# Kernel tuning notes

Measured on AMD Instinct MI355X. Metric: run time of the kernel, lower is better.

The kernel has to match this reference:

```python
import jax, jax.numpy as jnp
import numpy as np

B, S, D, F, E, DT, K = 4, 2048, 1024, 4096, 8, 256, 2


def setup_inputs() -> dict:
    key = jax.random.key(0)
    ks = jax.random.split(key, 8)
    scale_g = 1.0 / np.sqrt(D)
    scale_t = 1.0 / np.sqrt(DT)
    scale_1 = 1.0 / np.sqrt(D)
    scale_2 = 1.0 / np.sqrt(F)
    return {
        "inputs": jax.random.normal(ks[0], (B, S, D), dtype=jnp.float32),
        "task_param": jax.random.normal(ks[1], (B, 1, DT), dtype=jnp.float32),
        "Wg_in": jax.random.normal(ks[2], (D, E), dtype=jnp.float32) * scale_g,
        "bg_in": jnp.zeros((E,), dtype=jnp.float32),
        "Wg_task": jax.random.normal(ks[3], (DT, E), dtype=jnp.float32) * scale_t,
        "bg_task": jnp.zeros((E,), dtype=jnp.float32),
        "alpha": jnp.float32(0.5),
        "W1": jax.random.normal(ks[4], (E, D, F), dtype=jnp.float32) * scale_1,
        "b1": jnp.zeros((E, F), dtype=jnp.float32),
        "W2": jax.random.normal(ks[5], (E, F, D), dtype=jnp.float32) * scale_2,
        "b2": jnp.zeros((E, D), dtype=jnp.float32),
    }


def reference(inputs, task_param, Wg_in, bg_in, Wg_task, bg_task, alpha, W1, b1, W2, b2):
    # Gating: blend input-gate and task-gate logits ([B,1,E] broadcasts over S)
    input_logits = jnp.einsum('bsd,de->bse', inputs, Wg_in) + bg_in
    task_logits = jnp.einsum('btd,de->bte', task_param, Wg_task) + bg_task
    gate_logits = (1.0 - alpha) * input_logits + alpha * task_logits  # [B,S,E]

    topk_vals, selected = jax.lax.top_k(gate_logits, K)  # [B,S,K]

    # Load-balancing auxiliary loss (float32 softmax, as in the original)
    weights_softmax = jax.nn.softmax(gate_logits.astype(jnp.float32), axis=-1).astype(inputs.dtype)
    average_weight = jnp.mean(weights_softmax, axis=(0, 1))  # [E]
    onehot = jax.nn.one_hot(selected, E, dtype=inputs.dtype)  # [B,S,K,E]
    average_count = jnp.mean(onehot.sum(axis=2), axis=(0, 1))  # [E]
    l_aux = jnp.mean(average_weight * average_count) * E

    # Combine weights: softmax over the top-k gate values
    w = jax.nn.softmax(topk_vals.astype(jnp.float32), axis=-1).astype(inputs.dtype)  # [B,S,K]

    # Dense expert compute (same math as the per-expert gather/scatter loop)
    h = jax.nn.silu(jnp.einsum('bsd,edf->ebsf', inputs, W1) + b1[:, None, None, :])  # [E,B,S,F]
    expert_out = jnp.einsum('ebsf,efd->ebsd', h, W2) + b2[:, None, None, :]          # [E,B,S,D]

    picked = jnp.einsum('bske,ebsd->bskd', onehot, expert_out)  # [B,S,K,D]
    results = jnp.einsum('bsk,bskd->bsd', w, picked)            # [B,S,D]
    return results, l_aux.astype(jnp.float32)
```

## Files before the change

kernel.cpp:

```cpp
#include <hip/hip_runtime.h>

#define T_TOK 8192
#define D_DIM 1024
#define F_DIM 4096
#define E_EXP 8
#define DT_DIM 256
#define GBLK 256

#define A_XB   0u
#define A_WT   16777216u
#define A_H    83886080u
#define A_Y    226492416u
#define A_META 262144000u
#define A_W2T  262428928u
#define W2T_NEED (262428928ull + 67108864ull)
#define MO_FILL   0
#define MO_PB     64
#define MO_NT     128
#define MO_PARTP  256
#define MO_PARTC  8448
#define MO_TILEE  16640
#define MO_TILERB 17664
#define MO_ROUTEE 18688
#define MO_ROUTEW 84224
#define MO_TSLOT  149760
#define MO_PTOK   215296
#define META_BYTES 284928

using bf16x8 = __attribute__((ext_vector_type(8))) short;
using f32x4  = __attribute__((ext_vector_type(4))) float;
typedef unsigned short u16;

__device__ __forceinline__ u16 f2bf(float f) {
  union { float f; unsigned u; } v; v.f = f;
  unsigned r = v.u + 0x7FFFu + ((v.u >> 16) & 1u);
  return (u16)(r >> 16);
}
__device__ __forceinline__ float bf2f(u16 h) {
  union { unsigned u; float f; } v; v.u = ((unsigned)h) << 16; return v.f;
}
__device__ __forceinline__ void gload16(const void* gsrc, void* ldst) {
  __builtin_amdgcn_global_load_lds(
      (const __attribute__((address_space(1))) void*)gsrc,
      (__attribute__((address_space(3))) void*)ldst, 16, 0, 0);
}

__device__ __forceinline__ void tcvt64_body(const float* __restrict__ src,
                                            u16* __restrict__ dst, int R, int C,
                                            int e, int rb, int cb, char* smem) {
  u16 (*tile)[65] = (u16(*)[65])smem;
  size_t off = (size_t)e * R * C;
  int t = threadIdx.x;
  int r = t >> 4, cq = (t & 15) << 2;
#pragma unroll
  for (int k = 0; k < 4; k++) {
    int rr = r + k * 16;
    float4 v = *(const float4*)(src + off + (size_t)(rb + rr) * C + cb + cq);
    tile[rr][cq] = f2bf(v.x);
    tile[rr][cq + 1] = f2bf(v.y);
    tile[rr][cq + 2] = f2bf(v.z);
    tile[rr][cq + 3] = f2bf(v.w);
  }
  __syncthreads();
  int r4 = (t & 15) << 2, c0 = t >> 4;
#pragma unroll
  for (int j = 0; j < 4; j++) {
    int c = c0 + j * 16;
    ushort4 o;
    o.x = tile[r4][c]; o.y = tile[r4 + 1][c];
    o.z = tile[r4 + 2][c]; o.w = tile[r4 + 3][c];
    *(ushort4*)(dst + off + (size_t)(cb + c) * R + rb + r4) = o;
  }
}

__global__ __launch_bounds__(256) void prep(
    const float* __restrict__ X, const float* __restrict__ TP,
    const float* __restrict__ Wg, const float* __restrict__ bg,
    const float* __restrict__ Wt, const float* __restrict__ bgt,
    const float* __restrict__ alphaP,
    const float* __restrict__ W1,
    u16* __restrict__ Xb, u16* __restrict__ W1T, int* meta) {
  __shared__ char smem[41216];
  int bid = blockIdx.x;
  if (bid >= GBLK) {
    int loc = bid - GBLK;
    int e = loc >> 10, t10 = loc & 1023;
    tcvt64_body(W1, W1T, D_DIM, F_DIM, e, (t10 & 15) << 6, (t10 >> 4) << 6, smem);
    return;
  }
  float* WgT = (float*)smem;
  float* WtT = (float*)(smem + 32768);
  float* wsP = (float*)(smem + 40960);
  int*   wsC = (int*)(smem + 41088);
  int tid = threadIdx.x;
  for (int i = tid; i < E_EXP * D_DIM; i += 256) { int d = i >> 3, e = i & 7; WgT[e * D_DIM + d] = Wg[i]; }
  for (int i = tid; i < E_EXP * DT_DIM; i += 256) { int d = i >> 3, e = i & 7; WtT[e * DT_DIM + d] = Wt[i]; }
  __syncthreads();
  int lane = tid & 63, wid = tid >> 6;
  int tb = bid * 32;
  int b = tb >> 11;
  float alpha = alphaP[0];

  float tac[8] = {};
#pragma unroll
  for (int i = 0; i < 4; i++) {
    int d = lane + i * 64;
    float x = TP[b * DT_DIM + d];
#pragma unroll
    for (int e = 0; e < 8; e++) tac[e] += x * WtT[e * DT_DIM + d];
  }
  for (int off = 32; off > 0; off >>= 1)
#pragma unroll
    for (int e = 0; e < 8; e++) tac[e] += __shfl_xor(tac[e], off);
  float tl[8];
#pragma unroll
  for (int e = 0; e < 8; e++) tl[e] = alpha * (tac[e] + bgt[e]);

  float psum[8] = {};
  int   cnt[8] = {};
  for (int i = 0; i < 8; i++) {
    int t = tb + wid * 8 + i;
    const float* xr = X + (size_t)t * D_DIM;
    float acc[8] = {};
    u16 xb[16];
#pragma unroll 4
    for (int j = 0; j < 16; j++) {
      int d = lane + j * 64;
      float x = xr[d];
      xb[j] = f2bf(x);
#pragma unroll
      for (int e = 0; e < 8; e++) acc[e] += x * WgT[e * D_DIM + d];
    }
#pragma unroll
    for (int j = 0; j < 16; j++) Xb[(size_t)t * D_DIM + lane + j * 64] = xb[j];
    for (int off = 32; off > 0; off >>= 1)
#pragma unroll
      for (int e = 0; e < 8; e++) acc[e] += __shfl_xor(acc[e], off);
    float gl[8];
#pragma unroll
    for (int e = 0; e < 8; e++) gl[e] = (1.f - alpha) * (acc[e] + bg[e]) + tl[e];
    int e1 = 0;
#pragma unroll
    for (int e = 1; e < 8; e++) if (gl[e] > gl[e1]) e1 = e;
    int es = (e1 == 0) ? 1 : 0;
#pragma unroll
    for (int e = 0; e < 8; e++) if (e != e1 && gl[e] > gl[es]) es = e;
    float mx = gl[0];
#pragma unroll
    for (int e = 1; e < 8; e++) mx = fmaxf(mx, gl[e]);
    float pe[8], se = 0.f;
#pragma unroll
    for (int e = 0; e < 8; e++) { pe[e] = __expf(gl[e] - mx); se += pe[e]; }
    float inv = 1.f / se;
    if (lane == 0) {
#pragma unroll
      for (int e = 0; e < 8; e++) psum[e] += pe[e] * inv;
      cnt[e1]++; cnt[es]++;
      float w1 = 1.f / (1.f + __expf(gl[es] - gl[e1]));
      meta[MO_ROUTEE / 4 + 2 * t] = e1;
      meta[MO_ROUTEE / 4 + 2 * t + 1] = es;
      ((float*)meta)[MO_ROUTEW / 4 + 2 * t] = w1;
      ((float*)meta)[MO_ROUTEW / 4 + 2 * t + 1] = 1.f - w1;
    }
  }
  if (lane == 0) {
#pragma unroll
    for (int e = 0; e < 8; e++) { wsP[wid * 8 + e] = psum[e]; wsC[wid * 8 + e] = cnt[e]; }
  }
  __syncthreads();
  if (tid < 8) {
    float p = wsP[tid] + wsP[8 + tid] + wsP[16 + tid] + wsP[24 + tid];
    int   c = wsC[tid] + wsC[8 + tid] + wsC[16 + tid] + wsC[24 + tid];
    ((float*)meta)[MO_PARTP / 4 + bid * 8 + tid] = p;
    meta[MO_PARTC / 4 + bid * 8 + tid] = c;
  }
}

__global__ __launch_bounds__(256) void tcvt2k(const float* __restrict__ W2,
                                              u16* __restrict__ W2T) {
  __shared__ char smem[8448];
  int loc = blockIdx.x;
  int e = loc >> 10, t10 = loc & 1023;
  tcvt64_body(W2, W2T, F_DIM, D_DIM, e, (t10 >> 4) << 6, (t10 & 15) << 6, smem);
}

__global__ void plan(int* meta, float* out) {
  __shared__ float sp[8];
  __shared__ int   sc[8];
  int tid = threadIdx.x;
  if (blockIdx.x != 0) return;
  if (tid < 8) {
    const float* pp = (const float*)meta + MO_PARTP / 4;
    const int*   pc = meta + MO_PARTC / 4;
    float p = 0.f; int c = 0;
    for (int b = 0; b < GBLK; b++) { p += pp[b * 8 + tid]; c += pc[b * 8 + tid]; }
    sp[tid] = p; sc[tid] = c;
    meta[MO_FILL / 4 + tid] = 0;
  }
  int* ptok = meta + MO_PTOK / 4;
  for (int i = tid; i < 17408; i += 64) ptok[i] = 0;
  __syncthreads();
  if (tid == 0) {
    int* pb = meta + MO_PB / 4;
    int* tileE = meta + MO_TILEE / 4;
    int* tileRB = meta + MO_TILERB / 4;
    int base = 0, nt = 0;
    float la = 0.f;
    for (int e = 0; e < 8; e++) {
      int n = sc[e];
      pb[e] = base;
      int ntl = (n + 127) >> 7;
      for (int i = 0; i < ntl; i++) { tileE[nt] = e; tileRB[nt] = base + (i << 7); nt++; }
      base += ntl << 7;
      la += (sp[e] * (1.f / 8192.f)) * ((float)n * (1.f / 8192.f));
    }
    pb[8] = base;
    meta[MO_NT / 4] = nt;
    out[T_TOK * D_DIM] = la;
  }
}

__global__ __launch_bounds__(256) void fillk(int* meta) {
  int t = blockIdx.x * 256 + threadIdx.x;
  int lane = threadIdx.x & 63;
  int* pb = meta + MO_PB / 4;
  int* fl = meta + MO_FILL / 4;
  int* ptok = meta + MO_PTOK / 4;
  int* ts = meta + MO_TSLOT / 4;
  unsigned long long lmask = (1ull << lane) - 1;
#pragma unroll
  for (int k = 0; k < 2; k++) {
    int e = meta[MO_ROUTEE / 4 + 2 * t + k];
    int slot = 0;
    for (int ee = 0; ee < 8; ee++) {
      unsigned long long mask = __ballot(e == ee);
      if (e == ee) {
        int low = __ffsll((long long)mask) - 1;
        int pre = __popcll(mask & lmask);
        int base = 0;
        if (lane == low) base = atomicAdd(&fl[ee], __popcll(mask));
        base = __shfl(base, low);
        slot = pb[ee] + base + pre;
      }
    }
    ptok[slot] = t;
    ts[2 * t + k] = slot;
  }
}


#define BUFA(i) ((char*)smem + (i) * 16384)
#define BUFB(i) ((char*)smem + (i) * 16384 + 8192)

__global__ __launch_bounds__(256) void gemm1(
    const u16* __restrict__ Xb, const u16* __restrict__ W1T,
    const float* __restrict__ b1, u16* __restrict__ H,
    const float* __restrict__ W2, u16* __restrict__ W2T,
    const int* __restrict__ meta) {
  __shared__ char smem[49152];
  if (blockIdx.x >= 4352) {
    int loc = blockIdx.x - 4352;
    int e = loc >> 10, t10 = loc & 1023;
    tcvt64_body(W2, W2T, F_DIM, D_DIM, e, (t10 >> 4) << 6, (t10 & 15) << 6, smem);
    return;
  }
  int xcd = blockIdx.x & 7, loc = blockIdx.x >> 3;
  int bt = loc >> 2;
  int cb = (xcd * 4 + (loc & 3)) * 128;
  int nt = meta[MO_NT / 4];
  if (bt >= nt) return;
  int e = meta[MO_TILEE / 4 + bt];
  int rb = meta[MO_TILERB / 4 + bt];
  const int* ptok = meta + MO_PTOK / 4;

  int tid = threadIdx.x, lane = tid & 63, wid = tid >> 6;
  int wr = wid >> 1, wc = wid & 1;
  int r0 = tid >> 2;
  int c0 = (((tid & 3) ^ ((r0 >> 1) & 3)) << 3);
  int tok0 = ptok[rb + r0];
  int tok1 = ptok[rb + r0 + 64];
  const u16* gA0 = Xb + (size_t)tok0 * D_DIM + c0;
  const u16* gA1 = Xb + (size_t)tok1 * D_DIM + c0;
  const u16* gB0 = W1T + ((size_t)e * F_DIM + cb + r0) * D_DIM + c0;
  const u16* gB1 = gB0 + (size_t)64 * D_DIM;

#define STAGE_G1(buf, k0)                                  \
  {                                                        \
    gload16(gA0 + (k0), BUFA(buf) + wid * 1024);           \
    gload16(gA1 + (k0), BUFA(buf) + 4096 + wid * 1024);    \
    gload16(gB0 + (k0), BUFB(buf) + wid * 1024);           \
    gload16(gB1 + (k0), BUFB(buf) + 4096 + wid * 1024);    \
  }

  f32x4 acc[4][4] = {};
  int kb = (((lane >> 4) ^ (((lane & 15) >> 1) & 3)) << 3);
  int ra = wr * 64 + (lane & 15);
  int rn = wc * 64 + (lane & 15);
  STAGE_G1(0, 0)
  STAGE_G1(1, 32)
  int cur = 0;
  for (int kt = 0; kt < 32; kt++) {
    if (kt + 1 < 32)
      asm volatile("s_waitcnt vmcnt(4) lgkmcnt(0)" ::: "memory");
    else
      asm volatile("s_waitcnt vmcnt(0) lgkmcnt(0)" ::: "memory");
    __builtin_amdgcn_sched_barrier(0);
    __builtin_amdgcn_s_barrier();
    int nxt = cur + 2; if (nxt >= 3) nxt -= 3;
    if (kt + 2 < 32) STAGE_G1(nxt, (kt + 2) * 32)
    const short* pA = (const short*)BUFA(cur);
    const short* pB = (const short*)BUFB(cur);
    bf16x8 af[4], bfr[4];
#pragma unroll
    for (int m = 0; m < 4; m++)
      af[m] = *(const bf16x8*)((const char*)pA + ((ra + m * 16) * 32 + kb) * 2);
#pragma unroll
    for (int n = 0; n < 4; n++)
      bfr[n] = *(const bf16x8*)((const char*)pB + ((rn + n * 16) * 32 + kb) * 2);
    __builtin_amdgcn_s_setprio(1);
#pragma unroll
    for (int m = 0; m < 4; m++)
#pragma unroll
      for (int n = 0; n < 4; n++)
        acc[m][n] = __builtin_amdgcn_mfma_f32_16x16x32_bf16(af[m], bfr[n], acc[m][n], 0, 0, 0);
    __builtin_amdgcn_s_setprio(0);
    cur = cur + 1 == 3 ? 0 : cur + 1;
  }
  int rbase = wr * 64 + ((lane >> 4) << 2);
  int cbase = cb + wc * 64 + (lane & 15);
#pragma unroll
  for (int m = 0; m < 4; m++)
#pragma unroll
    for (int n = 0; n < 4; n++) {
      int f = cbase + n * 16;
      float bias = b1[e * F_DIM + f];
#pragma unroll
      for (int r = 0; r < 4; r++) {
        int p = rb + rbase + m * 16 + r;
        float v = acc[m][n][r] + bias;
        float s = v * (1.0f / (1.0f + __expf(-v)));
        H[(size_t)p * F_DIM + f] = f2bf(s);
      }
    }
}

__global__ __launch_bounds__(256) void gemm2(
    const u16* __restrict__ H, const u16* __restrict__ W2T,
    const float* __restrict__ b2, u16* __restrict__ Y, const int* __restrict__ meta) {
  __shared__ char smem[49152];
  int id = blockIdx.x;
  int wg = (id & 7) * 136 + (id >> 3);
  int bt = wg >> 3;
  int cb = (wg & 7) * 128;
  int nt = meta[MO_NT / 4];
  if (bt >= nt) return;
  int e = meta[MO_TILEE / 4 + bt];
  int rb = meta[MO_TILERB / 4 + bt];
  int tid = threadIdx.x, lane = tid & 63, wid = tid >> 6;
  int wr = wid >> 1, wc = wid & 1;
  int r0 = tid >> 2;
  int c0 = (((tid & 3) ^ ((r0 >> 1) & 3)) << 3);
  const u16* gA0 = H + (size_t)(rb + r0) * F_DIM + c0;
  const u16* gA1 = gA0 + (size_t)64 * F_DIM;
  const u16* gB0 = W2T + ((size_t)e * D_DIM + cb + r0) * F_DIM + c0;
  const u16* gB1 = gB0 + (size_t)64 * F_DIM;

#define STAGE_G2(buf, k0)                                  \
  {                                                        \
    gload16(gA0 + (k0), BUFA(buf) + wid * 1024);           \
    gload16(gA1 + (k0), BUFA(buf) + 4096 + wid * 1024);    \
    gload16(gB0 + (k0), BUFB(buf) + wid * 1024);           \
    gload16(gB1 + (k0), BUFB(buf) + 4096 + wid * 1024);    \
  }

  f32x4 acc[4][4] = {};
  int kb = (((lane >> 4) ^ (((lane & 15) >> 1) & 3)) << 3);
  int ra = wr * 64 + (lane & 15);
  int rn = wc * 64 + (lane & 15);
  STAGE_G2(0, 0)
  STAGE_G2(1, 32)
  int cur = 0;
  for (int kt = 0; kt < 128; kt++) {
    if (kt + 1 < 128)
      asm volatile("s_waitcnt vmcnt(4) lgkmcnt(0)" ::: "memory");
    else
      asm volatile("s_waitcnt vmcnt(0) lgkmcnt(0)" ::: "memory");
    __builtin_amdgcn_sched_barrier(0);
    __builtin_amdgcn_s_barrier();
    int nxt = cur + 2; if (nxt >= 3) nxt -= 3;
    if (kt + 2 < 128) STAGE_G2(nxt, (kt + 2) * 32)
    const short* pA = (const short*)BUFA(cur);
    const short* pB = (const short*)BUFB(cur);
    bf16x8 af[4], bfr[4];
#pragma unroll
    for (int m = 0; m < 4; m++)
      af[m] = *(const bf16x8*)((const char*)pA + ((ra + m * 16) * 32 + kb) * 2);
#pragma unroll
    for (int n = 0; n < 4; n++)
      bfr[n] = *(const bf16x8*)((const char*)pB + ((rn + n * 16) * 32 + kb) * 2);
    __builtin_amdgcn_s_setprio(1);
#pragma unroll
    for (int m = 0; m < 4; m++)
#pragma unroll
      for (int n = 0; n < 4; n++)
        acc[m][n] = __builtin_amdgcn_mfma_f32_16x16x32_bf16(af[m], bfr[n], acc[m][n], 0, 0, 0);
    __builtin_amdgcn_s_setprio(0);
    cur = cur + 1 == 3 ? 0 : cur + 1;
  }
  int rbase = wr * 64 + ((lane >> 4) << 2);
  int cbase = cb + wc * 64 + (lane & 15);
#pragma unroll
  for (int m = 0; m < 4; m++)
#pragma unroll
    for (int n = 0; n < 4; n++) {
      int d = cbase + n * 16;
      float bias = b2[e * D_DIM + d];
#pragma unroll
      for (int r = 0; r < 4; r++) {
        int p = rb + rbase + m * 16 + r;
        Y[(size_t)p * D_DIM + d] = f2bf(acc[m][n][r] + bias);
      }
    }
}

__global__ __launch_bounds__(256) void combine(const u16* __restrict__ Y,
                                               const int* __restrict__ meta,
                                               float* __restrict__ out) {
  int t = blockIdx.x;
  const int* ts = meta + MO_TSLOT / 4;
  const float* rw = (const float*)meta + MO_ROUTEW / 4;
  int s1 = ts[2 * t], s2 = ts[2 * t + 1];
  float w1 = rw[2 * t], w2 = rw[2 * t + 1];
  int d0 = threadIdx.x * 4;
  ushort4 a = *(const ushort4*)(Y + (size_t)s1 * D_DIM + d0);
  ushort4 b = *(const ushort4*)(Y + (size_t)s2 * D_DIM + d0);
  float4 v;
  v.x = w1 * bf2f(a.x) + w2 * bf2f(b.x);
  v.y = w1 * bf2f(a.y) + w2 * bf2f(b.y);
  v.z = w1 * bf2f(a.z) + w2 * bf2f(b.z);
  v.w = w1 * bf2f(a.w) + w2 * bf2f(b.w);
  *(float4*)(out + (size_t)t * D_DIM + d0) = v;
}

extern "C" void kernel_launch(void* const* d_in, const int* in_sizes, int n_in,
                              void* d_out, int out_size, void* d_ws, size_t ws_size,
                              hipStream_t stream) {
  (void)in_sizes; (void)n_in; (void)out_size;
  const float* X    = (const float*)d_in[0];
  const float* TP   = (const float*)d_in[1];
  const float* Wg   = (const float*)d_in[2];
  const float* bg   = (const float*)d_in[3];
  const float* Wt   = (const float*)d_in[4];
  const float* bgt  = (const float*)d_in[5];
  const float* alp  = (const float*)d_in[6];
  const float* W1   = (const float*)d_in[7];
  const float* b1   = (const float*)d_in[8];
  const float* W2   = (const float*)d_in[9];
  const float* b2   = (const float*)d_in[10];
  float* out = (float*)d_out;
  char* ws = (char*)d_ws;
  u16* Xb = (u16*)(ws + A_XB);
  u16* WT = (u16*)(ws + A_WT);
  u16* H  = (u16*)(ws + A_H);
  u16* Y  = (u16*)(ws + A_Y);
  int* meta = (int*)(ws + A_META);

  int big = ws_size >= W2T_NEED;
  u16* W2T = big ? (u16*)(ws + A_W2T) : WT;

  prep<<<GBLK + 8192, 256, 0, stream>>>(X, TP, Wg, bg, Wt, bgt, alp, W1,
                                        Xb, WT, meta);
  plan<<<1, 64, 0, stream>>>(meta, out);
  fillk<<<T_TOK / 256, 256, 0, stream>>>(meta);
  gemm1<<<4352 + (big ? 8192 : 0), 256, 0, stream>>>(Xb, WT, b1, H, W2, W2T, meta);
  if (!big) tcvt2k<<<8192, 256, 0, stream>>>(W2, WT);
  gemm2<<<1088, 256, 0, stream>>>(H, W2T, b2, Y, meta);
  combine<<<T_TOK, 256, 0, stream>>>(Y, meta, out);
}
```

Before: 533.6 us.

## Use 256-row M tiles with 512-thread blocks in both expert GEMMs

Result: slower. 588.8 us (+10.3%).

```diff
diff --git a/kernel.cpp b/kernel.cpp
--- a/kernel.cpp
+++ b/kernel.cpp
@@ -6,6 +6,7 @@
 #define E_EXP 8
 #define DT_DIM 256
 #define GBLK 256
+#define NT256 76
 
 #define A_XB   0u
 #define A_WT   16777216u
@@ -47,10 +48,9 @@
 
 __device__ __forceinline__ void tcvt64_body(const float* __restrict__ src,
                                             u16* __restrict__ dst, int R, int C,
-                                            int e, int rb, int cb, char* smem) {
+                                            int e, int rb, int cb, char* smem, int t) {
   u16 (*tile)[65] = (u16(*)[65])smem;
   size_t off = (size_t)e * R * C;
-  int t = threadIdx.x;
   int r = t >> 4, cq = (t & 15) << 2;
 #pragma unroll
   for (int k = 0; k < 4; k++) {
@@ -85,7 +85,7 @@
   if (bid >= GBLK) {
     int loc = bid - GBLK;
     int e = loc >> 10, t10 = loc & 1023;
-    tcvt64_body(W1, W1T, D_DIM, F_DIM, e, (t10 & 15) << 6, (t10 >> 4) << 6, smem);
+    tcvt64_body(W1, W1T, D_DIM, F_DIM, e, (t10 & 15) << 6, (t10 >> 4) << 6, smem, threadIdx.x);
     return;
   }
   float* WgT = (float*)smem;
@@ -181,7 +181,7 @@
   __shared__ char smem[8448];
   int loc = blockIdx.x;
   int e = loc >> 10, t10 = loc & 1023;
-  tcvt64_body(W2, W2T, F_DIM, D_DIM, e, (t10 >> 4) << 6, (t10 & 15) << 6, smem);
+  tcvt64_body(W2, W2T, F_DIM, D_DIM, e, (t10 >> 4) << 6, (t10 & 15) << 6, smem, threadIdx.x);
 }
 
 __global__ void plan(int* meta, float* out) {
@@ -209,9 +209,10 @@
     for (int e = 0; e < 8; e++) {
       int n = sc[e];
       pb[e] = base;
-      int ntl = (n + 127) >> 7;
-      for (int i = 0; i < ntl; i++) { tileE[nt] = e; tileRB[nt] = base + (i << 7); nt++; }
-      base += ntl << 7;
+      int seg = ((n + 127) >> 7) << 7;
+      int ntl = (seg + 255) >> 8;
+      for (int i = 0; i < ntl; i++) { tileE[nt] = e; tileRB[nt] = base + (i << 8); nt++; }
+      base += seg;
       la += (sp[e] * (1.f / 8192.f)) * ((float)n * (1.f / 8192.f));
     }
     pb[8] = base;
@@ -249,67 +250,69 @@
 }
 
 
-#define BUFA(i) ((char*)smem + (i) * 16384)
-#define BUFB(i) ((char*)smem + (i) * 16384 + 8192)
-
-__global__ __launch_bounds__(256) void gemm1(
+#define BUF_A(i) (smem + (i) * 24576)
+#define BUF_B(i) (smem + (i) * 24576 + 16384)
+
+__global__ __launch_bounds__(512, 4) void gemm1(
     const u16* __restrict__ Xb, const u16* __restrict__ W1T,
     const float* __restrict__ b1, u16* __restrict__ H,
     const float* __restrict__ W2, u16* __restrict__ W2T,
     const int* __restrict__ meta) {
-  __shared__ char smem[49152];
-  if (blockIdx.x >= 4352) {
-    int loc = blockIdx.x - 4352;
-    int e = loc >> 10, t10 = loc & 1023;
-    tcvt64_body(W2, W2T, F_DIM, D_DIM, e, (t10 >> 4) << 6, (t10 & 15) << 6, smem);
+  __shared__ char smem[73728];
+  int tid = threadIdx.x;
+  if (blockIdx.x >= 2432) {
+    int pair = (blockIdx.x - 2432) * 2 + (tid >> 8);
+    int e = pair >> 10, t10 = pair & 1023;
+    tcvt64_body(W2, W2T, F_DIM, D_DIM, e, (t10 >> 4) << 6, (t10 & 15) << 6,
+                smem + (tid >> 8) * 8448, tid & 255);
     return;
   }
   int xcd = blockIdx.x & 7, loc = blockIdx.x >> 3;
-  int bt = loc >> 2;
-  int cb = (xcd * 4 + (loc & 3)) * 128;
+  int bt = loc % 76;
+  int cb = (xcd * 4 + loc / 76) * 128;
   int nt = meta[MO_NT / 4];
   if (bt >= nt) return;
   int e = meta[MO_TILEE / 4 + bt];
   int rb = meta[MO_TILERB / 4 + bt];
+  int rowEnd = meta[MO_PB / 4 + e + 1];
   const int* ptok = meta + MO_PTOK / 4;
 
-  int tid = threadIdx.x, lane = tid & 63, wid = tid >> 6;
+  int lane = tid & 63, wid = tid >> 6;
   int wr = wid >> 1, wc = wid & 1;
-  int r0 = tid >> 2;
-  int c0 = (((tid & 3) ^ ((r0 >> 1) & 3)) << 3);
-  int tok0 = ptok[rb + r0];
-  int tok1 = ptok[rb + r0 + 64];
-  const u16* gA0 = Xb + (size_t)tok0 * D_DIM + c0;
-  const u16* gA1 = Xb + (size_t)tok1 * D_DIM + c0;
-  const u16* gB0 = W1T + ((size_t)e * F_DIM + cb + r0) * D_DIM + c0;
-  const u16* gB1 = gB0 + (size_t)64 * D_DIM;
-
-#define STAGE_G1(buf, k0)                                  \
-  {                                                        \
-    gload16(gA0 + (k0), BUFA(buf) + wid * 1024);           \
-    gload16(gA1 + (k0), BUFA(buf) + 4096 + wid * 1024);    \
-    gload16(gB0 + (k0), BUFB(buf) + wid * 1024);           \
-    gload16(gB1 + (k0), BUFB(buf) + 4096 + wid * 1024);    \
+  int gcA = lane & 3;
+  int rA0 = wid * 32 + (lane >> 2), rA1 = rA0 + 16;
+  int i0 = rb + rA0; i0 = i0 < 17407 ? i0 : 17407;
+  int i1 = rb + rA1; i1 = i1 < 17407 ? i1 : 17407;
+  const u16* srcA0 = Xb + (size_t)ptok[i0] * D_DIM + ((gcA ^ ((rA0 >> 1) & 3)) << 3);
+  const u16* srcA1 = Xb + (size_t)ptok[i1] * D_DIM + ((gcA ^ ((rA1 >> 1) & 3)) << 3);
+  int rB = tid >> 2, gcB = tid & 3;
+  const u16* srcB = W1T + ((size_t)e * F_DIM + cb + rB) * D_DIM + ((gcB ^ ((rB >> 1) & 3)) << 3);
+
+#define STG1(buf, k0)                                        \
+  {                                                          \
+    gload16(srcA0 + (k0), BUF_A(buf) + wid * 2048);          \
+    gload16(srcA1 + (k0), BUF_A(buf) + wid * 2048 + 1024);   \
+    gload16(srcB + (k0), BUF_B(buf) + wid * 1024);           \
   }
 
   f32x4 acc[4][4] = {};
   int kb = (((lane >> 4) ^ (((lane & 15) >> 1) & 3)) << 3);
   int ra = wr * 64 + (lane & 15);
   int rn = wc * 64 + (lane & 15);
-  STAGE_G1(0, 0)
-  STAGE_G1(1, 32)
+  STG1(0, 0)
+  STG1(1, 32)
   int cur = 0;
   for (int kt = 0; kt < 32; kt++) {
     if (kt + 1 < 32)
-      asm volatile("s_waitcnt vmcnt(4) lgkmcnt(0)" ::: "memory");
+      asm volatile("s_waitcnt vmcnt(3) lgkmcnt(0)" ::: "memory");
     else
       asm volatile("s_waitcnt vmcnt(0) lgkmcnt(0)" ::: "memory");
     __builtin_amdgcn_sched_barrier(0);
     __builtin_amdgcn_s_barrier();
     int nxt = cur + 2; if (nxt >= 3) nxt -= 3;
-    if (kt + 2 < 32) STAGE_G1(nxt, (kt + 2) * 32)
-    const short* pA = (const short*)BUFA(cur);
-    const short* pB = (const short*)BUFB(cur);
+    if (kt + 2 < 32) STG1(nxt, (kt + 2) * 32)
+    const short* pA = (const short*)BUF_A(cur);
+    const short* pB = (const short*)BUF_B(cur);
     bf16x8 af[4], bfr[4];
 #pragma unroll
     for (int m = 0; m < 4; m++)
@@ -337,60 +340,66 @@
 #pragma unroll
       for (int r = 0; r < 4; r++) {
         int p = rb + rbase + m * 16 + r;
-        float v = acc[m][n][r] + bias;
-        float s = v * (1.0f / (1.0f + __expf(-v)));
-        H[(size_t)p * F_DIM + f] = f2bf(s);
+        if (p < rowEnd) {
+          float v = acc[m][n][r] + bias;
+          float s = v * (1.0f / (1.0f + __expf(-v)));
+          H[(size_t)p * F_DIM + f] = f2bf(s);
+        }
       }
     }
 }
 
-__global__ __launch_bounds__(256) void gemm2(
+__global__ __launch_bounds__(512, 4) void gemm2(
     const u16* __restrict__ H, const u16* __restrict__ W2T,
     const float* __restrict__ b2, u16* __restrict__ Y, const int* __restrict__ meta) {
-  __shared__ char smem[49152];
+  __shared__ char smem[73728];
+  int tid = threadIdx.x;
   int id = blockIdx.x;
-  int wg = (id & 7) * 136 + (id >> 3);
+  int wg = (id & 7) * 76 + (id >> 3);
   int bt = wg >> 3;
   int cb = (wg & 7) * 128;
   int nt = meta[MO_NT / 4];
   if (bt >= nt) return;
   int e = meta[MO_TILEE / 4 + bt];
   int rb = meta[MO_TILERB / 4 + bt];
-  int tid = threadIdx.x, lane = tid & 63, wid = tid >> 6;
+  int rowEnd = meta[MO_PB / 4 + e + 1];
+
+  int lane = tid & 63, wid = tid >> 6;
   int wr = wid >> 1, wc = wid & 1;
-  int r0 = tid >> 2;
-  int c0 = (((tid & 3) ^ ((r0 >> 1) & 3)) << 3);
-  const u16* gA0 = H + (size_t)(rb + r0) * F_DIM + c0;
-  const u16* gA1 = gA0 + (size_t)64 * F_DIM;
-  const u16* gB0 = W2T + ((size_t)e * D_DIM + cb + r0) * F_DIM + c0;
-  const u16* gB1 = gB0 + (size_t)64 * F_DIM;
-
-#define STAGE_G2(buf, k0)                                  \
-  {                                                        \
-    gload16(gA0 + (k0), BUFA(buf) + wid * 1024);           \
-    gload16(gA1 + (k0), BUFA(buf) + 4096 + wid * 1024);    \
-    gload16(gB0 + (k0), BUFB(buf) + wid * 1024);           \
-    gload16(gB1 + (k0), BUFB(buf) + 4096 + wid * 1024);    \
+  int gcA = lane & 3;
+  int rA0 = wid * 32 + (lane >> 2), rA1 = rA0 + 16;
+  int i0 = rb + rA0; i0 = i0 < 17407 ? i0 : 17407;
+  int i1 = rb + rA1; i1 = i1 < 17407 ? i1 : 17407;
+  const u16* srcA0 = H + (size_t)i0 * F_DIM + ((gcA ^ ((rA0 >> 1) & 3)) << 3);
+  const u16* srcA1 = H + (size_t)i1 * F_DIM + ((gcA ^ ((rA1 >> 1) & 3)) << 3);
+  int rB = tid >> 2, gcB = tid & 3;
+  const u16* srcB = W2T + ((size_t)e * D_DIM + cb + rB) * F_DIM + ((gcB ^ ((rB >> 1) & 3)) << 3);
+
+#define STG2(buf, k0)                                        \
+  {                                                          \
+    gload16(srcA0 + (k0), BUF_A(buf) + wid * 2048);          \
+    gload16(srcA1 + (k0), BUF_A(buf) + wid * 2048 + 1024);   \
+    gload16(srcB + (k0), BUF_B(buf) + wid * 1024);           \
   }
 
   f32x4 acc[4][4] = {};
   int kb = (((lane >> 4) ^ (((lane & 15) >> 1) & 3)) << 3);
   int ra = wr * 64 + (lane & 15);
   int rn = wc * 64 + (lane & 15);
-  STAGE_G2(0, 0)
-  STAGE_G2(1, 32)
+  STG2(0, 0)
+  STG2(1, 32)
   int cur = 0;
   for (int kt = 0; kt < 128; kt++) {
     if (kt + 1 < 128)
-      asm volatile("s_waitcnt vmcnt(4) lgkmcnt(0)" ::: "memory");
+      asm volatile("s_waitcnt vmcnt(3) lgkmcnt(0)" ::: "memory");
     else
       asm volatile("s_waitcnt vmcnt(0) lgkmcnt(0)" ::: "memory");
     __builtin_amdgcn_sched_barrier(0);
     __builtin_amdgcn_s_barrier();
     int nxt = cur + 2; if (nxt >= 3) nxt -= 3;
-    if (kt + 2 < 128) STAGE_G2(nxt, (kt + 2) * 32)
-    const short* pA = (const short*)BUFA(cur);
-    const short* pB = (const short*)BUFB(cur);
+    if (kt + 2 < 128) STG2(nxt, (kt + 2) * 32)
+    const short* pA = (const short*)BUF_A(cur);
+    const short* pB = (const short*)BUF_B(cur);
     bf16x8 af[4], bfr[4];
 #pragma unroll
     for (int m = 0; m < 4; m++)
@@ -418,7 +427,8 @@
 #pragma unroll
       for (int r = 0; r < 4; r++) {
         int p = rb + rbase + m * 16 + r;
-        Y[(size_t)p * D_DIM + d] = f2bf(acc[m][n][r] + bias);
+        if (p < rowEnd)
+          Y[(size_t)p * D_DIM + d] = f2bf(acc[m][n][r] + bias);
       }
     }
 }
@@ -472,8 +482,8 @@
                                         Xb, WT, meta);
   plan<<<1, 64, 0, stream>>>(meta, out);
   fillk<<<T_TOK / 256, 256, 0, stream>>>(meta);
-  gemm1<<<4352 + (big ? 8192 : 0), 256, 0, stream>>>(Xb, WT, b1, H, W2, W2T, meta);
+  gemm1<<<2432 + (big ? 4096 : 0), 512, 0, stream>>>(Xb, WT, b1, H, W2, W2T, meta);
   if (!big) tcvt2k<<<8192, 256, 0, stream>>>(W2, WT);
-  gemm2<<<1088, 256, 0, stream>>>(H, W2T, b2, Y, meta);
+  gemm2<<<608, 512, 0, stream>>>(H, W2T, b2, Y, meta);
   combine<<<T_TOK, 256, 0, stream>>>(Y, meta, out);
 }
```

## Fuse expert-output combine into gemm2 epilogue via weighted atomic adds

Applied to the files above, without the earlier changes.

Result: slower. 570.4 us (+6.9%).

```diff
diff --git a/kernel.cpp b/kernel.cpp
--- a/kernel.cpp
+++ b/kernel.cpp
@@ -12,8 +12,8 @@
 #define A_H    83886080u
 #define A_Y    226492416u
 #define A_META 262144000u
-#define A_W2T  262428928u
-#define W2T_NEED (262428928ull + 67108864ull)
+#define A_W2T  262498560u
+#define W2T_NEED (262498560ull + 67108864ull)
 #define MO_FILL   0
 #define MO_PB     64
 #define MO_NT     128
@@ -25,7 +25,8 @@
 #define MO_ROUTEW 84224
 #define MO_TSLOT  149760
 #define MO_PTOK   215296
-#define META_BYTES 284928
+#define MO_WSLOT  284928
+#define META_BYTES 354560
 
 using bf16x8 = __attribute__((ext_vector_type(8))) short;
 using f32x4  = __attribute__((ext_vector_type(4))) float;
@@ -79,9 +80,16 @@
     const float* __restrict__ Wt, const float* __restrict__ bgt,
     const float* __restrict__ alphaP,
     const float* __restrict__ W1,
-    u16* __restrict__ Xb, u16* __restrict__ W1T, int* meta) {
+    u16* __restrict__ Xb, u16* __restrict__ W1T, int* meta,
+    float* __restrict__ out) {
   __shared__ char smem[41216];
   int bid = blockIdx.x;
+  if (bid >= GBLK + 8192) {
+    size_t base = (size_t)(bid - GBLK - 8192) * 2048 + threadIdx.x * 4;
+    *(float4*)(out + base) = make_float4(0.f, 0.f, 0.f, 0.f);
+    *(float4*)(out + base + 1024) = make_float4(0.f, 0.f, 0.f, 0.f);
+    return;
+  }
   if (bid >= GBLK) {
     int loc = bid - GBLK;
     int e = loc >> 10, t10 = loc & 1023;
@@ -198,7 +206,8 @@
     meta[MO_FILL / 4 + tid] = 0;
   }
   int* ptok = meta + MO_PTOK / 4;
-  for (int i = tid; i < 17408; i += 64) ptok[i] = 0;
+  float* wsl = (float*)meta + MO_WSLOT / 4;
+  for (int i = tid; i < 17408; i += 64) { ptok[i] = 0; wsl[i] = 0.f; }
   __syncthreads();
   if (tid == 0) {
     int* pb = meta + MO_PB / 4;
@@ -227,6 +236,7 @@
   int* fl = meta + MO_FILL / 4;
   int* ptok = meta + MO_PTOK / 4;
   int* ts = meta + MO_TSLOT / 4;
+  float* wsl = (float*)meta + MO_WSLOT / 4;
   unsigned long long lmask = (1ull << lane) - 1;
 #pragma unroll
   for (int k = 0; k < 2; k++) {
@@ -245,6 +255,7 @@
     }
     ptok[slot] = t;
     ts[2 * t + k] = slot;
+    wsl[slot] = ((const float*)meta)[MO_ROUTEW / 4 + 2 * t + k];
   }
 }
 
@@ -346,7 +357,8 @@
 
 __global__ __launch_bounds__(256) void gemm2(
     const u16* __restrict__ H, const u16* __restrict__ W2T,
-    const float* __restrict__ b2, u16* __restrict__ Y, const int* __restrict__ meta) {
+    const float* __restrict__ b2, float* __restrict__ out,
+    const int* __restrict__ meta) {
   __shared__ char smem[49152];
   int id = blockIdx.x;
   int wg = (id & 7) * 136 + (id >> 3);
@@ -409,37 +421,23 @@
   }
   int rbase = wr * 64 + ((lane >> 4) << 2);
   int cbase = cb + wc * 64 + (lane & 15);
+  const int* ptok = meta + MO_PTOK / 4;
+  const float* wsl = (const float*)meta + MO_WSLOT / 4;
+  float bias[4];
+#pragma unroll
+  for (int n = 0; n < 4; n++) bias[n] = b2[e * D_DIM + cbase + n * 16];
 #pragma unroll
   for (int m = 0; m < 4; m++)
 #pragma unroll
-    for (int n = 0; n < 4; n++) {
-      int d = cbase + n * 16;
-      float bias = b2[e * D_DIM + d];
-#pragma unroll
-      for (int r = 0; r < 4; r++) {
-        int p = rb + rbase + m * 16 + r;
-        Y[(size_t)p * D_DIM + d] = f2bf(acc[m][n][r] + bias);
-      }
-    }
-}
-
-__global__ __launch_bounds__(256) void combine(const u16* __restrict__ Y,
-                                               const int* __restrict__ meta,
-                                               float* __restrict__ out) {
-  int t = blockIdx.x;
-  const int* ts = meta + MO_TSLOT / 4;
-  const float* rw = (const float*)meta + MO_ROUTEW / 4;
-  int s1 = ts[2 * t], s2 = ts[2 * t + 1];
-  float w1 = rw[2 * t], w2 = rw[2 * t + 1];
-  int d0 = threadIdx.x * 4;
-  ushort4 a = *(const ushort4*)(Y + (size_t)s1 * D_DIM + d0);
-  ushort4 b = *(const ushort4*)(Y + (size_t)s2 * D_DIM + d0);
-  float4 v;
-  v.x = w1 * bf2f(a.x) + w2 * bf2f(b.x);
-  v.y = w1 * bf2f(a.y) + w2 * bf2f(b.y);
-  v.z = w1 * bf2f(a.z) + w2 * bf2f(b.z);
-  v.w = w1 * bf2f(a.w) + w2 * bf2f(b.w);
-  *(float4*)(out + (size_t)t * D_DIM + d0) = v;
+    for (int r = 0; r < 4; r++) {
+      int p = rb + rbase + m * 16 + r;
+      int tok = ptok[p];
+      float w = wsl[p];
+      float* orow = out + (size_t)tok * D_DIM + cbase;
+#pragma unroll
+      for (int n = 0; n < 4; n++)
+        atomicAdd(orow + n * 16, w * (acc[m][n][r] + bias[n]));
+    }
 }
 
 extern "C" void kernel_launch(void* const* d_in, const int* in_sizes, int n_in,
@@ -462,18 +460,16 @@
   u16* Xb = (u16*)(ws + A_XB);
   u16* WT = (u16*)(ws + A_WT);
   u16* H  = (u16*)(ws + A_H);
-  u16* Y  = (u16*)(ws + A_Y);
   int* meta = (int*)(ws + A_META);
 
   int big = ws_size >= W2T_NEED;
   u16* W2T = big ? (u16*)(ws + A_W2T) : WT;
 
-  prep<<<GBLK + 8192, 256, 0, stream>>>(X, TP, Wg, bg, Wt, bgt, alp, W1,
-                                        Xb, WT, meta);
+  prep<<<GBLK + 8192 + 4096, 256, 0, stream>>>(X, TP, Wg, bg, Wt, bgt, alp, W1,
+                                               Xb, WT, meta, out);
   plan<<<1, 64, 0, stream>>>(meta, out);
   fillk<<<T_TOK / 256, 256, 0, stream>>>(meta);
   gemm1<<<4352 + (big ? 8192 : 0), 256, 0, stream>>>(Xb, WT, b1, H, W2, W2T, meta);
   if (!big) tcvt2k<<<8192, 256, 0, stream>>>(W2, WT);
-  gemm2<<<1088, 256, 0, stream>>>(H, W2T, b2, Y, meta);
-  combine<<<T_TOK, 256, 0, stream>>>(Y, meta, out);
-}
+  gemm2<<<1088, 256, 0, stream>>>(H, W2T, b2, out, meta);
+}
```
